# Optimization experiments

Measured on AMD Instinct MI355X. Metric: run time of the kernel, lower is better.

Reference implementation:

```python
import jax, jax.numpy as jnp
import numpy as np

N, E = 50000, 800000
H, C_IN, C_HID, C_OUT = 4, 256, 64, 64
NEG_SLOPE = 0.2


def leaky_relu(x, s=NEG_SLOPE):
    return jnp.where(x >= 0, x, s * x)


def gat_conv(x, src, dst, W, att_src, att_dst, bias, n_nodes):
    # x: [N, F_in], W: [F_in, H*C], att_*: [1, H, C], bias: [H*C]
    Hh, Cc = att_src.shape[1], att_src.shape[2]
    h = (x @ W).reshape(n_nodes, Hh, Cc)            # [N, H, C]
    a_src = (h * att_src).sum(-1)                   # [N, H]
    a_dst = (h * att_dst).sum(-1)                   # [N, H]
    alpha = leaky_relu(a_src[src] + a_dst[dst])     # [E, H]
    # segment softmax over incoming edges of each destination node
    m = jax.ops.segment_max(alpha, dst, num_segments=n_nodes)   # [N, H]
    e = jnp.exp(alpha - m[dst])                     # [E, H]
    denom = jax.ops.segment_sum(e, dst, num_segments=n_nodes)   # [N, H]
    w = e / jnp.clip(denom, 1e-16)[dst]             # [E, H]
    out = jax.ops.segment_sum(w[:, :, None] * h[src], dst, num_segments=n_nodes)
    return out.reshape(n_nodes, Hh * Cc) + bias


def setup_inputs() -> dict:
    key = jax.random.key(0)
    ks = jax.random.split(key, 10)
    glorot = lambda k, shp: jax.random.normal(k, shp, jnp.float32) * np.sqrt(2.0 / (shp[0] + shp[-1]))
    return {
        "x": jax.random.normal(ks[0], (N, C_IN), jnp.float32),
        "edge_index": jax.random.randint(ks[1], (2, E), 0, N, jnp.int32),
        "W1": glorot(ks[2], (C_IN, H * C_HID)),
        "att_src1": glorot(ks[3], (1, H, C_HID)),
        "att_dst1": glorot(ks[4], (1, H, C_HID)),
        "b1": jnp.zeros((H * C_HID,), jnp.float32),
        "W2": glorot(ks[5], (H * C_HID, H * C_OUT)),
        "att_src2": glorot(ks[6], (1, H, C_OUT)),
        "att_dst2": glorot(ks[7], (1, H, C_OUT)),
        "b2": jnp.zeros((H * C_OUT,), jnp.float32),
    }


def reference(x, edge_index, W1, att_src1, att_dst1, b1, W2, att_src2, att_dst2, b2):
    n = x.shape[0]
    loops = jnp.arange(n, dtype=edge_index.dtype)
    src = jnp.concatenate([edge_index[0], loops])
    dst = jnp.concatenate([edge_index[1], loops])
    h1 = gat_conv(x, src, dst, W1, att_src1, att_dst1, b1, n)
    h1 = jax.nn.relu(h1)
    out = gat_conv(h1, src, dst, W2, att_src2, att_dst2, b2, n)
    return out
```

## Files before the change

kernel.cpp:

```cpp
#include <hip/hip_runtime.h>
#include <math.h>

#define NEG_SLOPE 0.2f

typedef __attribute__((ext_vector_type(8))) short bf16x8;
typedef __attribute__((ext_vector_type(4))) float f32x4;
typedef __attribute__((ext_vector_type(4))) unsigned short u16x4;
typedef __attribute__((ext_vector_type(8))) unsigned short u16x8;

static __device__ __forceinline__ f32x4 lky4(f32x4 v) {
    f32x4 r;
    r.x = v.x >= 0.f ? v.x : NEG_SLOPE * v.x;
    r.y = v.y >= 0.f ? v.y : NEG_SLOPE * v.y;
    r.z = v.z >= 0.f ? v.z : NEG_SLOPE * v.z;
    r.w = v.w >= 0.f ? v.w : NEG_SLOPE * v.w;
    return r;
}
static __device__ __forceinline__ f32x4 exp4(f32x4 v) {
    f32x4 r;
    r.x = __expf(v.x); r.y = __expf(v.y); r.z = __expf(v.z); r.w = __expf(v.w);
    return r;
}
static __device__ __forceinline__ float bf2f(unsigned short u) {
    return __uint_as_float(((unsigned int)u) << 16);
}
static __device__ __forceinline__ unsigned short f2bf_rne(float f) {
    unsigned int u = __float_as_uint(f);
    u += 0x7fffu + ((u >> 16) & 1u);
    return (unsigned short)(u >> 16);
}


__global__ void hist_kernel(const int* __restrict__ dst, int* __restrict__ counts, int E, int Nn) {
    int i = blockIdx.x * blockDim.x + threadIdx.x;
    int tot = E + Nn;
    if (i < tot) {
        int d = (i < E) ? dst[i] : (i - E);
        atomicAdd(&counts[d], 1);
    }
}

__global__ void scan1_kernel(const int* __restrict__ counts, int* __restrict__ partial,
                             int* __restrict__ blockSums, int Nn) {
    __shared__ int sh[1024];
    int b = blockIdx.x, t = threadIdx.x;
    int base = b * 1024;
    int orig[4];
    for (int r = 0; r < 4; r++) {
        int i = t + r * 256;
        int v = (base + i < Nn) ? counts[base + i] : 0;
        orig[r] = v;
        sh[i] = v;
    }
    __syncthreads();
    for (int off = 1; off < 1024; off <<= 1) {
        int vals[4];
        for (int r = 0; r < 4; r++) { int i = t + r * 256; vals[r] = (i >= off) ? sh[i - off] : 0; }
        __syncthreads();
        for (int r = 0; r < 4; r++) { int i = t + r * 256; sh[i] += vals[r]; }
        __syncthreads();
    }
    for (int r = 0; r < 4; r++) {
        int i = t + r * 256;
        if (base + i < Nn) partial[base + i] = sh[i] - orig[r];
    }
    if (t == 0) blockSums[b] = sh[1023];
}

__global__ void finalize_kernel(const int* __restrict__ partial, const int* __restrict__ blockSums,
                                int* __restrict__ row_ptr, int* __restrict__ counts,
                                int Nn, int Etot, int nb) {
    __shared__ int sh[64];
    int t = threadIdx.x;
    if (t < 64) {
        int v = (t < nb) ? blockSums[t] : 0;
        int orig = v;
#pragma unroll
        for (int off = 1; off < 64; off <<= 1) {
            int u = __shfl_up(v, off);
            if (t >= off) v += u;
        }
        sh[t] = v - orig;
    }
    __syncthreads();
    int i = blockIdx.x * blockDim.x + t;
    if (i < Nn) {
        row_ptr[i] = partial[i] + sh[i >> 10];
        counts[i] = 0;
    }
    if (i == 0) row_ptr[Nn] = Etot;
}

__global__ void scatter_kernel(const int* __restrict__ srcE, const int* __restrict__ dstE,
                               const int* __restrict__ row_ptr, int* __restrict__ fill,
                               int* __restrict__ srcs, int E, int Nn) {
    int i = blockIdx.x * blockDim.x + threadIdx.x;
    int tot = E + Nn;
    if (i < tot) {
        int s, d;
        if (i < E) { s = srcE[i]; d = dstE[i]; }
        else       { s = d = i - E; }
        int pos = row_ptr[d] + atomicAdd(&fill[d], 1);
        srcs[pos] = s;
    }
}

__global__ void prep_kernel(const float* __restrict__ X, unsigned short* __restrict__ Ab,
                            const float* __restrict__ W1, unsigned short* __restrict__ Bt1,
                            const float* __restrict__ W2, unsigned short* __restrict__ Bt2,
                            int rows, int nConv) {
    int b = blockIdx.x;
    if (b < nConv) {
        int t = b * 256 + threadIdx.x;
        if (t >= rows * 64) return;
        int r = t >> 6, c4 = t & 63;
        f32x4 v = *((const f32x4*)(X + ((size_t)r << 8)) + c4);
        u16x4 o;
        o.x = f2bf_rne(v.x); o.y = f2bf_rne(v.y);
        o.z = f2bf_rne(v.z); o.w = f2bf_rne(v.w);
        *(u16x4*)(Ab + (size_t)r * 256 + c4 * 4) = o;
    } else {
        int b2 = b - nConv;
        const float* W = (b2 < 256) ? W1 : W2;
        unsigned short* Bt = (b2 < 256) ? Bt1 : Bt2;
        int bb = (b2 < 256) ? b2 : b2 - 256;
        int t = bb * 256 + threadIdx.x;
        int n = t >> 8, k = t & 255;
        Bt[(size_t)n * 256 + k] = f2bf_rne(W[k * 256 + n]);
    }
}

__global__ __launch_bounds__(256) void gemm_kernel(const unsigned short* __restrict__ Ab,
                                                   const unsigned short* __restrict__ Bt,
                                                   unsigned short* __restrict__ Gb,
                                                   int rows, int nwg) {
    int orig = blockIdx.x;
    int q = nwg >> 3, r8 = nwg & 7;
    int xcd = orig & 7, idx = orig >> 3;
    int logical = (xcd < r8 ? xcd * (q + 1) : r8 * (q + 1) + (xcd - r8) * q) + idx;
    int bm = (logical >> 1) * 128;
    int bn = (logical & 1) * 128;

    __shared__ __align__(128) unsigned char smem[65536];

    int tid = threadIdx.x;
    int lane = tid & 63, wid = tid >> 6;
    int wr = wid >> 1, wc = wid & 1;

    f32x4 zero4 = {0.f, 0.f, 0.f, 0.f};
    f32x4 acc[4][4];
#pragma unroll
    for (int i = 0; i < 4; i++)
#pragma unroll
        for (int j = 0; j < 4; j++) acc[i][j] = zero4;

    int sr = tid >> 3;
    int sc = tid & 7;

    auto stage = [&](int kt, int buf) {
        unsigned short* As = (unsigned short*)(smem + buf * 32768);
        unsigned short* Bs = As + 8192;
#pragma unroll
        for (int q2 = 0; q2 < 4; q2++) {
            int rt = q2 * 32 + sr;
            int gr = bm + rt; if (gr >= rows) gr = rows - 1;
            int cg = sc ^ (rt & 7);
            const unsigned short* gp = Ab + (size_t)gr * 256 + kt + cg * 8;
            unsigned short* lp = As + rt * 64 + sc * 8;
            __builtin_amdgcn_global_load_lds(
                (__attribute__((address_space(1))) void*)(uintptr_t)gp,
                (__attribute__((address_space(3))) void*)lp, 16, 0, 0);
        }
#pragma unroll
        for (int q2 = 0; q2 < 4; q2++) {
            int rt = q2 * 32 + sr;
            int gn = bn + rt;
            int cg = sc ^ (rt & 7);
            const unsigned short* gp = Bt + (size_t)gn * 256 + kt + cg * 8;
            unsigned short* lp = Bs + rt * 64 + sc * 8;
            __builtin_amdgcn_global_load_lds(
                (__attribute__((address_space(1))) void*)(uintptr_t)gp,
                (__attribute__((address_space(3))) void*)lp, 16, 0, 0);
        }
    };

    stage(0, 0);
    __syncthreads();

    for (int kt = 0; kt < 4; kt++) {
        if (kt < 3) stage((kt + 1) * 64, (kt + 1) & 1);
        unsigned short* As = (unsigned short*)(smem + (kt & 1) * 32768);
        unsigned short* Bs = As + 8192;
#pragma unroll
        for (int ks = 0; ks < 2; ks++) {
            bf16x8 af[4], bfr[4];
#pragma unroll
            for (int f = 0; f < 4; f++) {
                int r = wr * 64 + f * 16 + (lane & 15);
                int c = (ks * 4 + (lane >> 4)) ^ (r & 7);
                af[f] = *(const bf16x8*)(As + r * 64 + c * 8);
                int rb = wc * 64 + f * 16 + (lane & 15);
                int cb = (ks * 4 + (lane >> 4)) ^ (rb & 7);
                bfr[f] = *(const bf16x8*)(Bs + rb * 64 + cb * 8);
            }
#pragma unroll
            for (int i = 0; i < 4; i++)
#pragma unroll
                for (int j = 0; j < 4; j++)
                    acc[i][j] = __builtin_amdgcn_mfma_f32_16x16x32_bf16(af[i], bfr[j], acc[i][j], 0, 0, 0);
        }
        __syncthreads();
    }

    int r0 = wr * 64 + (lane >> 4) * 4;
    int c0 = wc * 64 + (lane & 15);
#pragma unroll
    for (int i = 0; i < 4; i++) {
#pragma unroll
        for (int j = 0; j < 4; j++) {
#pragma unroll
            for (int rg = 0; rg < 4; rg++) {
                int lr = bm + r0 + i * 16 + rg;
                if (lr < rows) {
                    int col = bn + c0 + j * 16;
                    Gb[(size_t)lr * 256 + col] = f2bf_rne(acc[i][j][rg]);
                }
            }
        }
    }
}

__global__ __launch_bounds__(256) void attn_kernel(const unsigned short* __restrict__ Gb,
                                                   const float* __restrict__ att_s,
                                                   const float* __restrict__ att_d,
                                                   float* __restrict__ a_src,
                                                   float* __restrict__ a_dst, int N) {
    int wv = threadIdx.x >> 6, lane = threadIdx.x & 63;
    int n = blockIdx.x * 4 + wv;
    if (n >= N) return;
    u16x4 g4 = *(const u16x4*)(Gb + (size_t)n * 256 + lane * 4);
    f32x4 g;
    g.x = bf2f(g4.x); g.y = bf2f(g4.y); g.z = bf2f(g4.z); g.w = bf2f(g4.w);
    f32x4 s4 = ((const f32x4*)att_s)[lane];
    f32x4 d4 = ((const f32x4*)att_d)[lane];
    f32x4 p = g * s4, q = g * d4;
    float ps = p.x + p.y + p.z + p.w;
    float pd = q.x + q.y + q.z + q.w;
#pragma unroll
    for (int off = 1; off < 16; off <<= 1) {
        ps += __shfl_xor(ps, off);
        pd += __shfl_xor(pd, off);
    }
    if ((lane & 15) == 0) {
        int head = lane >> 4;
        a_src[n * 4 + head] = ps;
        a_dst[n * 4 + head] = pd;
    }
}

__global__ __launch_bounds__(64) void gather_kernel(const unsigned short* __restrict__ Gb,
                                                    const float* __restrict__ a_src,
                                                    const float* __restrict__ a_dst,
                                                    const int* __restrict__ row_ptr,
                                                    const int* __restrict__ srcs,
                                                    const float* __restrict__ bias,
                                                    float* __restrict__ outF,
                                                    unsigned short* __restrict__ outB,
                                                    int N) {
    __shared__ int s_lds[64];
    __shared__ f32x4 w_lds[64];
    int lane = threadIdx.x;
    int n = blockIdx.x;
    if (n >= N) return;
    int half = lane >> 5;
    int sl = lane & 31;
    int head = sl >> 3;

    int start = row_ptr[n], end = row_ptr[n + 1];
    const f32x4* as4p = (const f32x4*)a_src;
    f32x4 adn4 = *(const f32x4*)(a_dst + (size_t)n * 4);

    float acc[8] = {0.f, 0.f, 0.f, 0.f, 0.f, 0.f, 0.f, 0.f};
    f32x4 dsum4 = {0.f, 0.f, 0.f, 0.f};

    for (int c0 = start; c0 < end; c0 += 64) {
        int cnt = min(64, end - c0);
        if (lane < cnt) {
            int s = srcs[c0 + lane];
            f32x4 ev = exp4(lky4(as4p[s] + adn4));
            s_lds[lane] = s;
            w_lds[lane] = ev;
            dsum4 += ev;
        }

        int j = 0;
        for (; j + 7 < cnt; j += 8) {
            int sv_[4]; float wv_[4];
#pragma unroll
            for (int t = 0; t < 4; t++) {
                int e = j + 2 * t + half;
                sv_[t] = s_lds[e];
                wv_[t] = ((const float*)&w_lds[e])[head];
            }
            u16x8 gv_[4];
#pragma unroll
            for (int t = 0; t < 4; t++)
                gv_[t] = *(const u16x8*)(Gb + (size_t)sv_[t] * 256 + sl * 8);
#pragma unroll
            for (int t = 0; t < 4; t++)
#pragma unroll
                for (int k = 0; k < 8; k++)
                    acc[k] = fmaf(bf2f(gv_[t][k]), wv_[t], acc[k]);
        }
        for (; j < cnt; j += 2) {
            int e = j + half;
            if (e < cnt) {
                int s0 = s_lds[e];
                float w0 = ((const float*)&w_lds[e])[head];
                u16x8 g0 = *(const u16x8*)(Gb + (size_t)s0 * 256 + sl * 8);
#pragma unroll
                for (int k = 0; k < 8; k++)
                    acc[k] = fmaf(bf2f(g0[k]), w0, acc[k]);
            }
        }
    }

#pragma unroll
    for (int k = 0; k < 8; k++) acc[k] += __shfl_xor(acc[k], 32);
#pragma unroll
    for (int off = 32; off; off >>= 1) {
        dsum4.x += __shfl_xor(dsum4.x, off);
        dsum4.y += __shfl_xor(dsum4.y, off);
        dsum4.z += __shfl_xor(dsum4.z, off);
        dsum4.w += __shfl_xor(dsum4.w, off);
    }
    float den = head == 0 ? dsum4.x : head == 1 ? dsum4.y : head == 2 ? dsum4.z : dsum4.w;
    float rden = 1.0f / den;

    float r[8];
    const float* bp = bias + sl * 8;
#pragma unroll
    for (int k = 0; k < 8; k++) r[k] = acc[k] * rden + bp[k];

    if (outF) {
        if (half == 0) {
            f32x4 v0 = {r[0], r[1], r[2], r[3]};
            f32x4 v1 = {r[4], r[5], r[6], r[7]};
            f32x4* op = (f32x4*)(outF + (size_t)n * 256 + sl * 8);
            op[0] = v0; op[1] = v1;
        }
    } else {
        if (half == 0) {
            u16x8 v;
#pragma unroll
            for (int k = 0; k < 8; k++) v[k] = f2bf_rne(fmaxf(r[k], 0.f));
            *(u16x8*)(outB + (size_t)n * 256 + sl * 8) = v;
        }
    }
}


extern "C" void kernel_launch(void* const* d_in, const int* in_sizes, int n_in,
                              void* d_out, int out_size, void* d_ws, size_t ws_size,
                              hipStream_t stream) {
    const float* x   = (const float*)d_in[0];
    const int*   ei  = (const int*)d_in[1];
    const float* W1  = (const float*)d_in[2];
    const float* as1 = (const float*)d_in[3];
    const float* ad1 = (const float*)d_in[4];
    const float* b1  = (const float*)d_in[5];
    const float* W2  = (const float*)d_in[6];
    const float* as2 = (const float*)d_in[7];
    const float* ad2 = (const float*)d_in[8];
    const float* b2  = (const float*)d_in[9];

    int N = in_sizes[0] / 256;
    int E = in_sizes[1] / 2;
    int Etot = E + N;
    const int* srcE = ei;
    const int* dstE = ei + E;
    float* out = (float*)d_out;

    char* w = (char*)d_ws;
    size_t used = 0;
    auto alloc = [&](size_t bytes) -> char* {
        char* p = w + used;
        used += (bytes + 255) & ~(size_t)255;
        return p;
    };
    unsigned short* Gb = (unsigned short*)alloc((size_t)N * 256 * 2);
    unsigned short* Ab = (unsigned short*)alloc((size_t)N * 256 * 2);
    float* a_src   = (float*)alloc((size_t)N * 4 * 4);
    float* a_dst   = (float*)alloc((size_t)N * 4 * 4);
    int* counts    = (int*)alloc((size_t)N * 4);
    int* partial   = (int*)alloc((size_t)N * 4);
    int* row_ptr   = (int*)alloc(((size_t)N + 1) * 4);
    int* srcs      = (int*)alloc((size_t)Etot * 4);
    int* blockSums = (int*)alloc(256 * 4);
    unsigned short* Bt1 = (unsigned short*)alloc((size_t)256 * 256 * 2);
    unsigned short* Bt2 = (unsigned short*)alloc((size_t)256 * 256 * 2);

    hipMemsetAsync(counts, 0, (size_t)N * 4, stream);

    int nConv = (N * 64 + 255) / 256;
    prep_kernel<<<nConv + 512, 256, 0, stream>>>(x, Ab, W1, Bt1, W2, Bt2, N, nConv);

    hist_kernel<<<(Etot + 255) / 256, 256, 0, stream>>>(dstE, counts, E, N);
    int nScanBlocks = (N + 1023) / 1024;
    scan1_kernel<<<nScanBlocks, 256, 0, stream>>>(counts, partial, blockSums, N);
    finalize_kernel<<<(N + 255) / 256, 256, 0, stream>>>(partial, blockSums, row_ptr, counts,
                                                         N, Etot, nScanBlocks);
    scatter_kernel<<<(Etot + 255) / 256, 256, 0, stream>>>(srcE, dstE, row_ptr, counts, srcs, E, N);

    int nodeBlocks = (N + 3) / 4;
    int nwg = ((N + 127) / 128) * 2;

    gemm_kernel<<<nwg, 256, 0, stream>>>(Ab, Bt1, Gb, N, nwg);
    attn_kernel<<<nodeBlocks, 256, 0, stream>>>(Gb, as1, ad1, a_src, a_dst, N);
    gather_kernel<<<N, 64, 0, stream>>>(Gb, a_src, a_dst, row_ptr, srcs,
                                        b1, nullptr, Ab, N);

    gemm_kernel<<<nwg, 256, 0, stream>>>(Ab, Bt2, Gb, N, nwg);
    attn_kernel<<<nodeBlocks, 256, 0, stream>>>(Gb, as2, ad2, a_src, a_dst, N);
    gather_kernel<<<N, 64, 0, stream>>>(Gb, a_src, a_dst, row_ptr, srcs,
                                        b2, out, nullptr, N);
}
```

Before: 290.9 us.

## Single-buffer GEMM LDS and stage output tile through LDS for vectorized stores

```diff
diff --git a/kernel.cpp b/kernel.cpp
--- a/kernel.cpp
+++ b/kernel.cpp
@@ -141,7 +141,7 @@
     int bm = (logical >> 1) * 128;
     int bn = (logical & 1) * 128;
 
-    __shared__ __align__(128) unsigned char smem[65536];
+    __shared__ __align__(128) unsigned char smem[34816];
 
     int tid = threadIdx.x;
     int lane = tid & 63, wid = tid >> 6;
@@ -157,9 +157,11 @@
     int sr = tid >> 3;
     int sc = tid & 7;
 
-    auto stage = [&](int kt, int buf) {
-        unsigned short* As = (unsigned short*)(smem + buf * 32768);
-        unsigned short* Bs = As + 8192;
+    unsigned short* As = (unsigned short*)smem;
+    unsigned short* Bs = As + 8192;
+
+    for (int kt4 = 0; kt4 < 4; kt4++) {
+        int kt = kt4 * 64;
 #pragma unroll
         for (int q2 = 0; q2 < 4; q2++) {
             int rt = q2 * 32 + sr;
@@ -182,15 +184,7 @@
                 (__attribute__((address_space(1))) void*)(uintptr_t)gp,
                 (__attribute__((address_space(3))) void*)lp, 16, 0, 0);
         }
-    };
-
-    stage(0, 0);
-    __syncthreads();
-
-    for (int kt = 0; kt < 4; kt++) {
-        if (kt < 3) stage((kt + 1) * 64, (kt + 1) & 1);
-        unsigned short* As = (unsigned short*)(smem + (kt & 1) * 32768);
-        unsigned short* Bs = As + 8192;
+        __syncthreads();
 #pragma unroll
         for (int ks = 0; ks < 2; ks++) {
             bf16x8 af[4], bfr[4];
@@ -212,21 +206,27 @@
         __syncthreads();
     }
 
+    unsigned short* Cs = (unsigned short*)smem;
     int r0 = wr * 64 + (lane >> 4) * 4;
     int c0 = wc * 64 + (lane & 15);
 #pragma unroll
-    for (int i = 0; i < 4; i++) {
-#pragma unroll
-        for (int j = 0; j < 4; j++) {
-#pragma unroll
-            for (int rg = 0; rg < 4; rg++) {
-                int lr = bm + r0 + i * 16 + rg;
-                if (lr < rows) {
-                    int col = bn + c0 + j * 16;
-                    Gb[(size_t)lr * 256 + col] = f2bf_rne(acc[i][j][rg]);
-                }
-            }
-        }
+    for (int i = 0; i < 4; i++)
+#pragma unroll
+        for (int j = 0; j < 4; j++)
+#pragma unroll
+            for (int rg = 0; rg < 4; rg++)
+                Cs[(r0 + i * 16 + rg) * 136 + c0 + j * 16] = f2bf_rne(acc[i][j][rg]);
+    __syncthreads();
+
+    int row = tid >> 1;
+    int cb2 = (tid & 1) * 64;
+    int grow = bm + row;
+    if (grow < rows) {
+        unsigned short* dst = Gb + (size_t)grow * 256 + bn + cb2;
+        const unsigned short* src = Cs + row * 136 + cb2;
+#pragma unroll
+        for (int k = 0; k < 8; k++)
+            *(u16x8*)(dst + k * 8) = *(const u16x8*)(src + k * 8);
     }
 }
 
```

Result: slower. 300.5 us (+3.3%).
